# Performance work log

Hardware: AMD Instinct MI355X
Metric: run time of the kernel (lower is better)

Reference implementation:

```python
import jax, jax.numpy as jnp
import numpy as np

N_BASIS = 8
N_RANK = 4
IN_DIM = 64
B, T = 64, 8192


def _make_projections():
    # Match torch module: np.random.seed(15385); per rank draw E then F, QR, take first n_basis cols.
    np.random.seed(seed=15385)
    Es, Fs = [], []
    for _ in range(N_RANK):
        G = np.random.standard_normal([IN_DIM, IN_DIM])
        Q, _ = np.linalg.qr(G)
        Es.append(Q[:, :N_BASIS])
        G = np.random.standard_normal([IN_DIM, IN_DIM])
        Q, _ = np.linalg.qr(G)
        Fs.append(Q[:, :N_BASIS])
    E = jnp.asarray(np.stack(Es), dtype=jnp.float32)  # [R, C, nb]
    F = jnp.asarray(np.stack(Fs), dtype=jnp.float32)  # [R, C, nb]
    return E, F


def setup_inputs() -> dict:
    key = jax.random.key(0)
    x = jax.random.normal(key, (B, IN_DIM, T), dtype=jnp.float32)
    E, F = _make_projections()
    init_sigma = float(np.sqrt(IN_DIM))
    sigma = jnp.full((N_RANK,), init_sigma, dtype=jnp.float32)
    rho = jnp.full((N_RANK,), init_sigma, dtype=jnp.float32)
    return {"x": x, "sigma": sigma, "rho": rho, "E": E, "F": F}


def reference(x, sigma, rho, E, F):
    # x: [B, C, T]; E,F: [R, C, nb]; sigma,rho: [R]
    in_dim = x.shape[1]
    scale = jnp.sqrt(jnp.float32(in_dim))
    Er = (scale / (1e-05 + jnp.abs(sigma)))[:, None, None] * E  # [R, C, nb]
    Fr = (scale / (1e-05 + jnp.abs(rho)))[:, None, None] * F    # [R, C, nb]
    xe = jnp.einsum('bct,rcn->brtn', x, Er)  # [B, R, T, nb]
    xf = jnp.einsum('bct,rcm->brtm', x, Fr)  # [B, R, T, nb]
    # outer product per (b, t), summed over rank, averaged
    z = jnp.einsum('brtn,brtm->btnm', xe, xf) / jnp.float32(N_RANK)  # [B, T, nb, nb]
    bsz, tlen = x.shape[0], x.shape[2]
    out = z.reshape(bsz, tlen, N_BASIS * N_BASIS).transpose(0, 2, 1)  # [B, nb^2, T]
    # use_normalization=True: signed sqrt + channel max normalization
    out = jnp.sign(out) * (jnp.sqrt(jnp.abs(out) + 0.01) - jnp.float32(np.sqrt(0.01)))
    max_vals = jnp.max(jnp.abs(out), axis=1, keepdims=True)
    out = out / (max_vals + 1e-05)
    return out
```

## Files before the change

### kernel.cpp

```cpp
#include <hip/hip_runtime.h>

#define CC 64
#define TT 8192
#define NB 8
#define NW16 32768
#define GRID 768
#define NWAVES (GRID * 4)

typedef __attribute__((ext_vector_type(8))) short bf16x8;
typedef __attribute__((ext_vector_type(4))) float f32x4;
typedef __attribute__((ext_vector_type(4))) int i32x4;

union I4B8 { i32x4 i; bf16x8 b; };

__device__ __forceinline__ unsigned short f32_to_bf16_rn(float f) {
    unsigned u = __float_as_uint(f);
    unsigned r = (u + 0x7FFFu + ((u >> 16) & 1u)) >> 16;
    return (unsigned short)r;
}
__device__ __forceinline__ float bf16_to_f32(unsigned short h) {
    return __uint_as_float(((unsigned)h) << 16);
}

__global__ __launch_bounds__(256) void rpg_prep(
    const float* __restrict__ sigma, const float* __restrict__ rho,
    const float* __restrict__ E, const float* __restrict__ F,
    unsigned short* __restrict__ Wf)
{
    const int idx = blockIdx.x * 256 + threadIdx.x;
    if (idx >= 8192) return;
    const int j    = idx & 7;
    const int slot = idx >> 3;
    const int lane = slot & 63;
    const int h    = (slot >> 6) & 1;
    const int ks   = (slot >> 7) & 1;
    const int mt   = (slot >> 8) & 3;
    const int p = mt * 16 + (lane & 15);
    const int c = ks * 32 + (lane >> 4) * 8 + j;
    float val;
    if (p < 32) {
        const int r = p >> 3, n = p & 7;
        const float es = 8.0f / (1e-5f + fabsf(sigma[r]));
        const float fs = 8.0f / (1e-5f + fabsf(rho[r]));
        val = E[r * (CC * NB) + c * NB + n] * (es * fs * 0.25f);
    } else {
        const int r = (p - 32) >> 3, n = p & 7;
        val = F[r * (CC * NB) + c * NB + n];
    }
    const unsigned short hi = f32_to_bf16_rn(val);
    Wf[idx] = (h == 0) ? hi : f32_to_bf16_rn(val - bf16_to_f32(hi));
}

__global__ __launch_bounds__(256, 3) void rpg_main(
    const float* __restrict__ x,
    const unsigned short* __restrict__ Wf,
    float* __restrict__ out)
{
    const int tid  = threadIdx.x;
    const int w    = tid >> 6;
    const int lane = tid & 63;
    const int am   = lane & 15;
    const int ag   = lane >> 4;

    bf16x8 wfh[8], wfl[8];
    #pragma unroll
    for (int s = 0; s < 8; ++s) {
        wfh[s] = *(const bf16x8*)(Wf + ((s * 2 + 0) * 64 + lane) * 8);
        wfl[s] = *(const bf16x8*)(Wf + ((s * 2 + 1) * 64 + lane) * 8);
    }

    const bool ra0 = (ag & 2) == 0;
    const bool qlo = (ag & 1) == 0;

    int wid = blockIdx.x * 4 + w;

    float f[16];
    {
        const int b = wid >> 9, t0 = (wid & 511) << 4;
        const float* xp = x + b * (CC * TT) + t0 + am;
        #pragma unroll
        for (int k = 0; k < 16; ++k) {
            const int c = ((k >> 3) * 32) + ag * 8 + (k & 7);
            f[k] = xp[c * TT];
        }
    }

    #pragma unroll 1
    while (wid < NW16) {
        bf16x8 xh[2], xl[2];
        #pragma unroll
        for (int ks = 0; ks < 2; ++ks) {
            unsigned hw[4], lw[4];
            #pragma unroll
            for (int k = 0; k < 4; ++k) {
                const float f0 = f[ks * 8 + 2 * k];
                const float f1 = f[ks * 8 + 2 * k + 1];
                const unsigned u0 = __float_as_uint(f0), u1 = __float_as_uint(f1);
                hw[k] = (u0 >> 16) | (u1 & 0xFFFF0000u);
                const float h0 = __uint_as_float(u0 & 0xFFFF0000u);
                const float h1 = __uint_as_float(u1 & 0xFFFF0000u);
                lw[k] = (__float_as_uint(f0 - h0) >> 16) |
                        (__float_as_uint(f1 - h1) & 0xFFFF0000u);
            }
            I4B8 H, L;
            H.i = (i32x4){(int)hw[0], (int)hw[1], (int)hw[2], (int)hw[3]};
            L.i = (i32x4){(int)lw[0], (int)lw[1], (int)lw[2], (int)lw[3]};
            xh[ks] = H.b;
            xl[ks] = L.b;
        }

        const int b  = wid >> 9;
        const int t0 = (wid & 511) << 4;
        const int nxt = wid + NWAVES;

        if (nxt < NW16) {
            const int nb = nxt >> 9, nt0 = (nxt & 511) << 4;
            const float* xp = x + nb * (CC * TT) + nt0 + am;
            #pragma unroll
            for (int k = 0; k < 16; ++k) {
                const int c = ((k >> 3) * 32) + ag * 8 + (k & 7);
                f[k] = xp[c * TT];
            }
        }

        f32x4 acc[4];
        #pragma unroll
        for (int mt = 0; mt < 4; ++mt) {
            acc[mt] = (f32x4){0.0f, 0.0f, 0.0f, 0.0f};
            #pragma unroll
            for (int ks = 0; ks < 2; ++ks) {
                const bf16x8 wh = wfh[mt * 2 + ks];
                const bf16x8 wl = wfl[mt * 2 + ks];
                acc[mt] = __builtin_amdgcn_mfma_f32_16x16x32_bf16(wh, xh[ks], acc[mt], 0, 0, 0);
                acc[mt] = __builtin_amdgcn_mfma_f32_16x16x32_bf16(wh, xl[ks], acc[mt], 0, 0, 0);
                acc[mt] = __builtin_amdgcn_mfma_f32_16x16x32_bf16(wl, xh[ks], acc[mt], 0, 0, 0);
            }
        }

        float pA[4], pB[4], pC[4], pD[4];
        #pragma unroll
        for (int i = 0; i < 4; ++i) {
            pA[i] = __shfl_xor(acc[0][i], 32);
            pB[i] = __shfl_xor(acc[1][i], 32);
            pC[i] = __shfl_xor(acc[2][i], 32);
            pD[i] = __shfl_xor(acc[3][i], 32);
        }

        float xe_[4][2];
        #pragma unroll
        for (int e = 0; e < 2; ++e) {
            xe_[0][e] = ra0 ? acc[0][e] : pA[2 + e];
            xe_[1][e] = ra0 ? pA[e]     : acc[0][2 + e];
            xe_[2][e] = ra0 ? acc[1][e] : pB[2 + e];
            xe_[3][e] = ra0 ? pB[e]     : acc[1][2 + e];
        }

        float xfq0[4], xfq1[4], xfq2[4], xfq3[4];
        #pragma unroll
        for (int i = 0; i < 4; ++i) {
            xfq0[i] = ra0 ? acc[2][i] : pC[i];
            xfq1[i] = ra0 ? pC[i]     : acc[2][i];
            xfq2[i] = ra0 ? acc[3][i] : pD[i];
            xfq3[i] = ra0 ? pD[i]     : acc[3][i];
        }
        float xfo0[4], xfo1[4], xfo2[4], xfo3[4];
        #pragma unroll
        for (int i = 0; i < 4; ++i) {
            xfo0[i] = __shfl_xor(xfq0[i], 16);
            xfo1[i] = __shfl_xor(xfq1[i], 16);
            xfo2[i] = __shfl_xor(xfq2[i], 16);
            xfo3[i] = __shfl_xor(xfq3[i], 16);
        }
        float xfL[4][4], xfH[4][4];
        #pragma unroll
        for (int i = 0; i < 4; ++i) {
            xfL[0][i] = qlo ? xfq0[i] : xfo0[i];  xfH[0][i] = qlo ? xfo0[i] : xfq0[i];
            xfL[1][i] = qlo ? xfq1[i] : xfo1[i];  xfH[1][i] = qlo ? xfo1[i] : xfq1[i];
            xfL[2][i] = qlo ? xfq2[i] : xfo2[i];  xfH[2][i] = qlo ? xfo2[i] : xfq2[i];
            xfL[3][i] = qlo ? xfq3[i] : xfo3[i];  xfH[3][i] = qlo ? xfo3[i] : xfq3[i];
        }

        float z[2][8];
        float pm = 0.0f;
        #pragma unroll
        for (int e = 0; e < 2; ++e) {
            #pragma unroll
            for (int m = 0; m < 4; ++m) {
                float a = xe_[0][e] * xfL[0][m];
                a = fmaf(xe_[1][e], xfL[1][m], a);
                a = fmaf(xe_[2][e], xfL[2][m], a);
                a = fmaf(xe_[3][e], xfL[3][m], a);
                float s = __builtin_amdgcn_sqrtf(fabsf(a) + 0.01f) - 0.1f;
                float v = copysignf(s, a);
                z[e][m] = v;
                pm = fmaxf(pm, fabsf(v));
            }
            #pragma unroll
            for (int m = 0; m < 4; ++m) {
                float a = xe_[0][e] * xfH[0][m];
                a = fmaf(xe_[1][e], xfH[1][m], a);
                a = fmaf(xe_[2][e], xfH[2][m], a);
                a = fmaf(xe_[3][e], xfH[3][m], a);
                float s = __builtin_amdgcn_sqrtf(fabsf(a) + 0.01f) - 0.1f;
                float v = copysignf(s, a);
                z[e][4 + m] = v;
                pm = fmaxf(pm, fabsf(v));
            }
        }

        pm = fmaxf(pm, __shfl_xor(pm, 16));
        pm = fmaxf(pm, __shfl_xor(pm, 32));
        const float rinv = __builtin_amdgcn_rcpf(pm + 1e-5f);

        const int nbase = (qlo ? 0 : 4) + (ra0 ? 0 : 2);
        float* ob = out + b * (64 * TT) + t0 + am;
        #pragma unroll
        for (int e = 0; e < 2; ++e)
            #pragma unroll
            for (int m = 0; m < 8; ++m)
                ob[((nbase + e) * NB + m) * TT] = z[e][m] * rinv;

        wid = nxt;
    }
}

extern "C" void kernel_launch(void* const* d_in, const int* in_sizes, int n_in,
                              void* d_out, int out_size, void* d_ws, size_t ws_size,
                              hipStream_t stream) {
    const float* x     = (const float*)d_in[0];
    const float* sigma = (const float*)d_in[1];
    const float* rho   = (const float*)d_in[2];
    const float* E     = (const float*)d_in[3];
    const float* F     = (const float*)d_in[4];
    float* out = (float*)d_out;

    unsigned short* Wf = (unsigned short*)d_ws;

    rpg_prep<<<32, 256, 0, stream>>>(sigma, rho, E, F, Wf);

    rpg_main<<<GRID, 256, 0, stream>>>(x, Wf, out);
}
```

Baseline: 59.28 us.

## Fuse weight prep into main kernel via LDS and raise occupancy

Drops the separate prep kernel launch: each block builds the scaled hi/lo bf16 weight fragments in shared memory from sigma, rho, E and F, then reads them from LDS inside the MFMA loop instead of holding them in registers. Freeing those registers lets launch bounds rise to 4 blocks per SM, and the grid grows from 768 to 1024. The cost is redundant per-block prep work, a block barrier, and extra LDS reads every iteration.

```diff
diff --git a/kernel.cpp b/kernel.cpp
--- a/kernel.cpp
+++ b/kernel.cpp
@@ -4,7 +4,7 @@
 #define TT 8192
 #define NB 8
 #define NW16 32768
-#define GRID 768
+#define GRID 1024
 #define NWAVES (GRID * 4)
 
 typedef __attribute__((ext_vector_type(8))) short bf16x8;
@@ -22,51 +22,57 @@
     return __uint_as_float(((unsigned)h) << 16);
 }
 
-__global__ __launch_bounds__(256) void rpg_prep(
-    const float* __restrict__ sigma, const float* __restrict__ rho,
-    const float* __restrict__ E, const float* __restrict__ F,
-    unsigned short* __restrict__ Wf)
-{
-    const int idx = blockIdx.x * 256 + threadIdx.x;
-    if (idx >= 8192) return;
-    const int j    = idx & 7;
-    const int slot = idx >> 3;
-    const int lane = slot & 63;
-    const int h    = (slot >> 6) & 1;
-    const int ks   = (slot >> 7) & 1;
-    const int mt   = (slot >> 8) & 3;
-    const int p = mt * 16 + (lane & 15);
-    const int c = ks * 32 + (lane >> 4) * 8 + j;
-    float val;
-    if (p < 32) {
-        const int r = p >> 3, n = p & 7;
-        const float es = 8.0f / (1e-5f + fabsf(sigma[r]));
-        const float fs = 8.0f / (1e-5f + fabsf(rho[r]));
-        val = E[r * (CC * NB) + c * NB + n] * (es * fs * 0.25f);
-    } else {
-        const int r = (p - 32) >> 3, n = p & 7;
-        val = F[r * (CC * NB) + c * NB + n];
-    }
-    const unsigned short hi = f32_to_bf16_rn(val);
-    Wf[idx] = (h == 0) ? hi : f32_to_bf16_rn(val - bf16_to_f32(hi));
-}
-
-__global__ __launch_bounds__(256, 3) void rpg_main(
+__global__ __launch_bounds__(256, 4) void rpg_main(
     const float* __restrict__ x,
-    const unsigned short* __restrict__ Wf,
+    const float* __restrict__ sigma,
+    const float* __restrict__ rho,
+    const float* __restrict__ E,
+    const float* __restrict__ F,
     float* __restrict__ out)
 {
+    __shared__ __align__(16) char wsl[16384];
+
     const int tid  = threadIdx.x;
     const int w    = tid >> 6;
     const int lane = tid & 63;
     const int am   = lane & 15;
     const int ag   = lane >> 4;
 
-    bf16x8 wfh[8], wfl[8];
-    #pragma unroll
-    for (int s = 0; s < 8; ++s) {
-        wfh[s] = *(const bf16x8*)(Wf + ((s * 2 + 0) * 64 + lane) * 8);
-        wfl[s] = *(const bf16x8*)(Wf + ((s * 2 + 1) * 64 + lane) * 8);
+    {
+        const int r = tid >> 6;
+        const int c = tid & 63;
+        const float g = (8.0f / (1e-5f + fabsf(sigma[r]))) *
+                        (8.0f / (1e-5f + fabsf(rho[r]))) * 0.25f;
+        const int wks = c >> 5, wag = (c >> 3) & 3, wj = c & 7;
+        const float4 e0 = *(const float4*)(E + (r * 64 + c) * 8);
+        const float4 e1 = *(const float4*)(E + (r * 64 + c) * 8 + 4);
+        const float4 fv0 = *(const float4*)(F + (r * 64 + c) * 8);
+        const float4 fv1 = *(const float4*)(F + (r * 64 + c) * 8 + 4);
+        const float ev[8] = {e0.x, e0.y, e0.z, e0.w, e1.x, e1.y, e1.z, e1.w};
+        const float fv[8] = {fv0.x, fv0.y, fv0.z, fv0.w, fv1.x, fv1.y, fv1.z, fv1.w};
+        #pragma unroll
+        for (int n = 0; n < 8; ++n) {
+            {
+                const int p = r * 8 + n;
+                const float val = ev[n] * g;
+                const unsigned short hi = f32_to_bf16_rn(val);
+                const unsigned short lo = f32_to_bf16_rn(val - bf16_to_f32(hi));
+                const int mt = p >> 4, pam = p & 15;
+                char* base = wsl + ((((mt * 2 + wks) * 2 + 0) * 64 + wag * 16 + pam) << 4) + wj * 2;
+                *(unsigned short*)base = hi;
+                *(unsigned short*)(base + 1024) = lo;
+            }
+            {
+                const int p = 32 + r * 8 + n;
+                const float val = fv[n];
+                const unsigned short hi = f32_to_bf16_rn(val);
+                const unsigned short lo = f32_to_bf16_rn(val - bf16_to_f32(hi));
+                const int mt = p >> 4, pam = p & 15;
+                char* base = wsl + ((((mt * 2 + wks) * 2 + 0) * 64 + wag * 16 + pam) << 4) + wj * 2;
+                *(unsigned short*)base = hi;
+                *(unsigned short*)(base + 1024) = lo;
+            }
+        }
     }
 
     const bool ra0 = (ag & 2) == 0;
@@ -84,6 +90,8 @@
             f[k] = xp[c * TT];
         }
     }
+
+    __syncthreads();
 
     #pragma unroll 1
     while (wid < NW16) {
@@ -129,8 +137,9 @@
             acc[mt] = (f32x4){0.0f, 0.0f, 0.0f, 0.0f};
             #pragma unroll
             for (int ks = 0; ks < 2; ++ks) {
-                const bf16x8 wh = wfh[mt * 2 + ks];
-                const bf16x8 wl = wfl[mt * 2 + ks];
+                const int fb = ((mt * 2 + ks) * 2) * 1024 + lane * 16;
+                const bf16x8 wh = ((const I4B8*)(wsl + fb))->b;
+                const bf16x8 wl = ((const I4B8*)(wsl + fb + 1024))->b;
                 acc[mt] = __builtin_amdgcn_mfma_f32_16x16x32_bf16(wh, xh[ks], acc[mt], 0, 0, 0);
                 acc[mt] = __builtin_amdgcn_mfma_f32_16x16x32_bf16(wh, xl[ks], acc[mt], 0, 0, 0);
                 acc[mt] = __builtin_amdgcn_mfma_f32_16x16x32_bf16(wl, xh[ks], acc[mt], 0, 0, 0);
@@ -234,9 +243,5 @@
     const float* F     = (const float*)d_in[4];
     float* out = (float*)d_out;
 
-    unsigned short* Wf = (unsigned short*)d_ws;
-
-    rpg_prep<<<32, 256, 0, stream>>>(sigma, rho, E, F, Wf);
-
-    rpg_main<<<GRID, 256, 0, stream>>>(x, Wf, out);
-}
+    rpg_main<<<GRID, 256, 0, stream>>>(x, sigma, rho, E, F, out);
+}
```

Result: slower. 88.45 us (+49.2%).
